# Optimization experiments

Measured on AMD Instinct MI355X. Metric: run time of the kernel, lower is better.

Reference implementation:

```python
import jax, jax.numpy as jnp
import numpy as np

B, C, U, N = 8, 64, 3, 512


def setup_inputs() -> dict:
    key = jax.random.key(0)
    k1, k2, k3, k4 = jax.random.split(key, 4)
    x = jax.random.normal(k1, (B, C, U, N), dtype=jnp.float32)
    # nn.Linear weights [out, in], applied as x @ W.T over channel dim
    s = 1.0 / np.sqrt(C)
    Wq = jax.random.uniform(k2, (C, C), dtype=jnp.float32, minval=-s, maxval=s)
    Wk = jax.random.uniform(k3, (C, C), dtype=jnp.float32, minval=-s, maxval=s)
    Wv = jax.random.uniform(k4, (C, C), dtype=jnp.float32, minval=-s, maxval=s)
    return {"x": x, "Wq": Wq, "Wk": Wk, "Wv": Wv}


def reference(x, Wq, Wk, Wv):
    # VNLinear: Linear over channel dim (dim 1), no bias: out[b,d,u,n] = sum_c x[b,c,u,n] W[d,c]
    def vn_linear(t, W):
        return jnp.einsum('bcun,dc->bdun', t, W)

    q = vn_linear(x, Wq)
    k = vn_linear(x, Wk)
    v = vn_linear(x, Wv)
    scale = x.shape[1] ** (-0.5)  # in_channels^-0.5
    # contraction over tiny vector-neuron dim u=3
    attn_logits = jnp.einsum('bcui,bcuj->bcij', q, k) * scale  # [B,C,N,N]
    attn_weights = jax.nn.softmax(attn_logits, axis=-1)
    out = jnp.einsum('bcij,bcuj->bcui', attn_weights, v)  # [B,C,U,N]
    return x + out
```

## Files before the change

kernel.cpp:

```cpp
#include <hip/hip_runtime.h>

#define BB 8
#define CC 64
#define UU 3
#define NN 512
#define POS (UU * NN)
#define QKV_ELEMS (BB * CC * POS)
#define SCALE2 0.1803368801111793f

__global__ __launch_bounds__(256) void proj_kernel(
    const float* __restrict__ x,
    const float* __restrict__ Wq,
    const float* __restrict__ Wk,
    const float* __restrict__ Wv,
    float* __restrict__ ws)
{
    const int blk   = blockIdx.x;
    const int bd2   = blk / 6;
    const int chunk = blk % 6;
    const int b     = bd2 >> 5;
    const int d0    = (bd2 & 31) * 2;
    const int tid   = threadIdx.x;
    const int p     = chunk * 256 + tid;

    __shared__ float w[6][CC];
    if (tid < 128) {
        int r = tid >> 6, c = tid & 63;
        w[r][c]     = Wq[(d0 + r) * CC + c];
        w[2 + r][c] = Wk[(d0 + r) * CC + c];
        w[4 + r][c] = Wv[(d0 + r) * CC + c];
    }
    __syncthreads();

    const float* xb = x + (size_t)b * CC * POS + p;
    float q0 = 0.f, q1 = 0.f, k0 = 0.f, k1 = 0.f, v0 = 0.f, v1 = 0.f;
    #pragma unroll 8
    for (int c = 0; c < CC; ++c) {
        float xv = xb[c * POS];
        q0 = fmaf(xv, w[0][c], q0);
        q1 = fmaf(xv, w[1][c], q1);
        k0 = fmaf(xv, w[2][c], k0);
        k1 = fmaf(xv, w[3][c], k1);
        v0 = fmaf(xv, w[4][c], v0);
        v1 = fmaf(xv, w[5][c], v1);
    }

    float* qs = ws;
    float* ks = ws + QKV_ELEMS;
    float* vs = ws + 2 * QKV_ELEMS;
    size_t base = (size_t)(b * CC + d0) * POS + p;
    qs[base] = q0 * SCALE2;  qs[base + POS] = q1 * SCALE2;
    ks[base] = k0;           ks[base + POS] = k1;
    vs[base] = v0;           vs[base + POS] = v1;
}

__global__ __launch_bounds__(256) void attn_kernel(
    const float* __restrict__ x,
    const float* __restrict__ ws,
    float* __restrict__ out)
{
    const int blk  = blockIdx.x;
    const int bd   = blk >> 1;
    const int half = blk & 1;
    const int tid  = threadIdx.x;

    __shared__ float ks[UU][NN];
    __shared__ float vs[UU][NN];

    const float* qsg = ws + (size_t)bd * POS;
    const float* ksg = ws + QKV_ELEMS + (size_t)bd * POS;
    const float* vsg = ws + 2 * QKV_ELEMS + (size_t)bd * POS;

    float* ksf = &ks[0][0];
    float* vsf = &vs[0][0];
    for (int t = tid; t < POS; t += 256) {
        ksf[t] = ksg[t];
        vsf[t] = vsg[t];
    }
    __syncthreads();

    const int i  = half * 256 + tid;
    const float q0 = qsg[i];
    const float q1 = qsg[NN + i];
    const float q2 = qsg[2 * NN + i];

    float l = 0.f, a0 = 0.f, a1 = 0.f, a2 = 0.f;
    #pragma unroll 4
    for (int j = 0; j < NN; j += 4) {
        float4 k0 = *(const float4*)&ks[0][j];
        float4 k1 = *(const float4*)&ks[1][j];
        float4 k2 = *(const float4*)&ks[2][j];
        float4 v0 = *(const float4*)&vs[0][j];
        float4 v1 = *(const float4*)&vs[1][j];
        float4 v2 = *(const float4*)&vs[2][j];

        float s0 = fmaf(q0, k0.x, fmaf(q1, k1.x, q2 * k2.x));
        float s1 = fmaf(q0, k0.y, fmaf(q1, k1.y, q2 * k2.y));
        float s2 = fmaf(q0, k0.z, fmaf(q1, k1.z, q2 * k2.z));
        float s3 = fmaf(q0, k0.w, fmaf(q1, k1.w, q2 * k2.w));

        float p0 = __builtin_amdgcn_exp2f(s0);
        float p1 = __builtin_amdgcn_exp2f(s1);
        float p2 = __builtin_amdgcn_exp2f(s2);
        float p3 = __builtin_amdgcn_exp2f(s3);

        l += p0 + p1 + p2 + p3;
        a0 = fmaf(p0, v0.x, fmaf(p1, v0.y, fmaf(p2, v0.z, fmaf(p3, v0.w, a0))));
        a1 = fmaf(p0, v1.x, fmaf(p1, v1.y, fmaf(p2, v1.z, fmaf(p3, v1.w, a1))));
        a2 = fmaf(p0, v2.x, fmaf(p1, v2.y, fmaf(p2, v2.z, fmaf(p3, v2.w, a2))));
    }

    float inv = 1.0f / l;
    const float* xd = x + (size_t)bd * POS;
    float*       od = out + (size_t)bd * POS;
    od[i]           = xd[i]           + a0 * inv;
    od[NN + i]      = xd[NN + i]      + a1 * inv;
    od[2 * NN + i]  = xd[2 * NN + i]  + a2 * inv;
}

__global__ __launch_bounds__(256) void vn_attn_fused(
    const float* __restrict__ x,
    const float* __restrict__ Wq,
    const float* __restrict__ Wk,
    const float* __restrict__ Wv,
    float* __restrict__ out)
{
    const int bd  = blockIdx.x;
    const int b   = bd / CC;
    const int d   = bd % CC;
    const int tid = threadIdx.x;

    __shared__ float wq[CC], wk[CC], wv[CC];
    __shared__ float qs[UU][NN];
    __shared__ float ks[UU][NN];
    __shared__ float vs[UU][NN];

    if (tid < CC) {
        wq[tid] = Wq[d * CC + tid];
        wk[tid] = Wk[d * CC + tid];
        wv[tid] = Wv[d * CC + tid];
    }
    __syncthreads();

    const float* xb = x + (size_t)b * CC * POS;
    for (int p = tid; p < POS; p += 256) {
        float qa = 0.f, ka = 0.f, va = 0.f;
        #pragma unroll 8
        for (int c = 0; c < CC; ++c) {
            float xv = xb[c * POS + p];
            qa = fmaf(xv, wq[c], qa);
            ka = fmaf(xv, wk[c], ka);
            va = fmaf(xv, wv[c], va);
        }
        int u = p >> 9, n = p & (NN - 1);
        qs[u][n] = qa * SCALE2;
        ks[u][n] = ka;
        vs[u][n] = va;
    }
    __syncthreads();

    for (int i = tid; i < NN; i += 256) {
        float q0 = qs[0][i], q1 = qs[1][i], q2 = qs[2][i];
        float l = 0.f, a0 = 0.f, a1 = 0.f, a2 = 0.f;
        for (int j = 0; j < NN; j += 4) {
            float4 k0 = *(const float4*)&ks[0][j];
            float4 k1 = *(const float4*)&ks[1][j];
            float4 k2 = *(const float4*)&ks[2][j];
            float4 v0 = *(const float4*)&vs[0][j];
            float4 v1 = *(const float4*)&vs[1][j];
            float4 v2 = *(const float4*)&vs[2][j];
            float s0 = fmaf(q0, k0.x, fmaf(q1, k1.x, q2 * k2.x));
            float s1 = fmaf(q0, k0.y, fmaf(q1, k1.y, q2 * k2.y));
            float s2 = fmaf(q0, k0.z, fmaf(q1, k1.z, q2 * k2.z));
            float s3 = fmaf(q0, k0.w, fmaf(q1, k1.w, q2 * k2.w));
            float p0 = __builtin_amdgcn_exp2f(s0);
            float p1 = __builtin_amdgcn_exp2f(s1);
            float p2 = __builtin_amdgcn_exp2f(s2);
            float p3 = __builtin_amdgcn_exp2f(s3);
            l += p0 + p1 + p2 + p3;
            a0 = fmaf(p0, v0.x, fmaf(p1, v0.y, fmaf(p2, v0.z, fmaf(p3, v0.w, a0))));
            a1 = fmaf(p0, v1.x, fmaf(p1, v1.y, fmaf(p2, v1.z, fmaf(p3, v1.w, a1))));
            a2 = fmaf(p0, v2.x, fmaf(p1, v2.y, fmaf(p2, v2.z, fmaf(p3, v2.w, a2))));
        }
        float inv = 1.0f / l;
        size_t obase = ((size_t)(b * CC + d) * UU) * NN + i;
        const float* xd = xb + (size_t)d * POS;
        out[obase]          = xd[i]          + a0 * inv;
        out[obase + NN]     = xd[NN + i]     + a1 * inv;
        out[obase + 2 * NN] = xd[2 * NN + i] + a2 * inv;
    }
}

extern "C" void kernel_launch(void* const* d_in, const int* in_sizes, int n_in,
                              void* d_out, int out_size, void* d_ws, size_t ws_size,
                              hipStream_t stream) {
    const float* x  = (const float*)d_in[0];
    const float* Wq = (const float*)d_in[1];
    const float* Wk = (const float*)d_in[2];
    const float* Wv = (const float*)d_in[3];
    float* out = (float*)d_out;

    if (ws_size >= (size_t)3 * QKV_ELEMS * sizeof(float)) {
        float* ws = (float*)d_ws;
        proj_kernel<<<dim3(BB * 32 * 6), dim3(256), 0, stream>>>(x, Wq, Wk, Wv, ws);
        attn_kernel<<<dim3(BB * CC * 2), dim3(256), 0, stream>>>(x, ws, out);
    } else {
        vn_attn_fused<<<dim3(BB * CC), dim3(256), 0, stream>>>(x, Wq, Wk, Wv, out);
    }
}
```

Before: 110.7 us.

## Compute eight output channels per projection block and read K/V directly from global

```diff
diff --git a/kernel.cpp b/kernel.cpp
--- a/kernel.cpp
+++ b/kernel.cpp
@@ -16,42 +16,46 @@
     float* __restrict__ ws)
 {
     const int blk   = blockIdx.x;
-    const int bd2   = blk / 6;
+    const int bg    = blk / 6;
     const int chunk = blk % 6;
-    const int b     = bd2 >> 5;
-    const int d0    = (bd2 & 31) * 2;
+    const int b     = bg >> 3;
+    const int d0    = (bg & 7) * 8;
     const int tid   = threadIdx.x;
     const int p     = chunk * 256 + tid;
 
-    __shared__ float w[6][CC];
-    if (tid < 128) {
-        int r = tid >> 6, c = tid & 63;
-        w[r][c]     = Wq[(d0 + r) * CC + c];
-        w[2 + r][c] = Wk[(d0 + r) * CC + c];
-        w[4 + r][c] = Wv[(d0 + r) * CC + c];
+    __shared__ float w[24][CC];
+    for (int t = tid; t < 24 * CC; t += 256) {
+        int r = t >> 6, c = t & 63;
+        const float* W = (r < 8) ? Wq : (r < 16) ? Wk : Wv;
+        w[r][c] = W[(d0 + (r & 7)) * CC + c];
     }
     __syncthreads();
 
     const float* xb = x + (size_t)b * CC * POS + p;
-    float q0 = 0.f, q1 = 0.f, k0 = 0.f, k1 = 0.f, v0 = 0.f, v1 = 0.f;
-    #pragma unroll 8
+    float qa[8], ka[8], va[8];
+    #pragma unroll
+    for (int r = 0; r < 8; ++r) { qa[r] = 0.f; ka[r] = 0.f; va[r] = 0.f; }
+
     for (int c = 0; c < CC; ++c) {
         float xv = xb[c * POS];
-        q0 = fmaf(xv, w[0][c], q0);
-        q1 = fmaf(xv, w[1][c], q1);
-        k0 = fmaf(xv, w[2][c], k0);
-        k1 = fmaf(xv, w[3][c], k1);
-        v0 = fmaf(xv, w[4][c], v0);
-        v1 = fmaf(xv, w[5][c], v1);
+        #pragma unroll
+        for (int r = 0; r < 8; ++r) {
+            qa[r] = fmaf(xv, w[r][c],      qa[r]);
+            ka[r] = fmaf(xv, w[8 + r][c],  ka[r]);
+            va[r] = fmaf(xv, w[16 + r][c], va[r]);
+        }
     }
 
     float* qs = ws;
     float* ks = ws + QKV_ELEMS;
     float* vs = ws + 2 * QKV_ELEMS;
-    size_t base = (size_t)(b * CC + d0) * POS + p;
-    qs[base] = q0 * SCALE2;  qs[base + POS] = q1 * SCALE2;
-    ks[base] = k0;           ks[base + POS] = k1;
-    vs[base] = v0;           vs[base + POS] = v1;
+    #pragma unroll
+    for (int r = 0; r < 8; ++r) {
+        size_t base = (size_t)(b * CC + d0 + r) * POS + p;
+        qs[base] = qa[r] * SCALE2;
+        ks[base] = ka[r];
+        vs[base] = va[r];
+    }
 }
 
 __global__ __launch_bounds__(256) void attn_kernel(
@@ -63,36 +67,29 @@
     const int bd   = blk >> 1;
     const int half = blk & 1;
     const int tid  = threadIdx.x;
-
-    __shared__ float ks[UU][NN];
-    __shared__ float vs[UU][NN];
-
-    const float* qsg = ws + (size_t)bd * POS;
-    const float* ksg = ws + QKV_ELEMS + (size_t)bd * POS;
-    const float* vsg = ws + 2 * QKV_ELEMS + (size_t)bd * POS;
-
-    float* ksf = &ks[0][0];
-    float* vsf = &vs[0][0];
-    for (int t = tid; t < POS; t += 256) {
-        ksf[t] = ksg[t];
-        vsf[t] = vsg[t];
-    }
-    __syncthreads();
-
-    const int i  = half * 256 + tid;
+    const int i    = half * 256 + tid;
+
+    const float*  qsg = ws + (size_t)bd * POS;
+    const float4* k0p = (const float4*)(ws + QKV_ELEMS     + (size_t)bd * POS);
+    const float4* k1p = k0p + (NN / 4);
+    const float4* k2p = k0p + 2 * (NN / 4);
+    const float4* v0p = (const float4*)(ws + 2 * QKV_ELEMS + (size_t)bd * POS);
+    const float4* v1p = v0p + (NN / 4);
+    const float4* v2p = v0p + 2 * (NN / 4);
+
     const float q0 = qsg[i];
     const float q1 = qsg[NN + i];
     const float q2 = qsg[2 * NN + i];
 
     float l = 0.f, a0 = 0.f, a1 = 0.f, a2 = 0.f;
-    #pragma unroll 4
-    for (int j = 0; j < NN; j += 4) {
-        float4 k0 = *(const float4*)&ks[0][j];
-        float4 k1 = *(const float4*)&ks[1][j];
-        float4 k2 = *(const float4*)&ks[2][j];
-        float4 v0 = *(const float4*)&vs[0][j];
-        float4 v1 = *(const float4*)&vs[1][j];
-        float4 v2 = *(const float4*)&vs[2][j];
+    #pragma unroll 2
+    for (int j4 = 0; j4 < NN / 4; ++j4) {
+        float4 k0 = k0p[j4];
+        float4 k1 = k1p[j4];
+        float4 k2 = k2p[j4];
+        float4 v0 = v0p[j4];
+        float4 v1 = v1p[j4];
+        float4 v2 = v2p[j4];
 
         float s0 = fmaf(q0, k0.x, fmaf(q1, k1.x, q2 * k2.x));
         float s1 = fmaf(q0, k0.y, fmaf(q1, k1.y, q2 * k2.y));
@@ -104,18 +101,18 @@
         float p2 = __builtin_amdgcn_exp2f(s2);
         float p3 = __builtin_amdgcn_exp2f(s3);
 
-        l += p0 + p1 + p2 + p3;
+        l += (p0 + p1) + (p2 + p3);
         a0 = fmaf(p0, v0.x, fmaf(p1, v0.y, fmaf(p2, v0.z, fmaf(p3, v0.w, a0))));
         a1 = fmaf(p0, v1.x, fmaf(p1, v1.y, fmaf(p2, v1.z, fmaf(p3, v1.w, a1))));
         a2 = fmaf(p0, v2.x, fmaf(p1, v2.y, fmaf(p2, v2.z, fmaf(p3, v2.w, a2))));
     }
 
     float inv = 1.0f / l;
-    const float* xd = x + (size_t)bd * POS;
+    const float* xd = x   + (size_t)bd * POS;
     float*       od = out + (size_t)bd * POS;
-    od[i]           = xd[i]           + a0 * inv;
-    od[NN + i]      = xd[NN + i]      + a1 * inv;
-    od[2 * NN + i]  = xd[2 * NN + i]  + a2 * inv;
+    od[i]          = xd[i]          + a0 * inv;
+    od[NN + i]     = xd[NN + i]     + a1 * inv;
+    od[2 * NN + i] = xd[2 * NN + i] + a2 * inv;
 }
 
 __global__ __launch_bounds__(256) void vn_attn_fused(
@@ -202,7 +199,7 @@
 
     if (ws_size >= (size_t)3 * QKV_ELEMS * sizeof(float)) {
         float* ws = (float*)d_ws;
-        proj_kernel<<<dim3(BB * 32 * 6), dim3(256), 0, stream>>>(x, Wq, Wk, Wv, ws);
+        proj_kernel<<<dim3(8 * 8 * 6), dim3(256), 0, stream>>>(x, Wq, Wk, Wv, ws);
         attn_kernel<<<dim3(BB * CC * 2), dim3(256), 0, stream>>>(x, ws, out);
     } else {
         vn_attn_fused<<<dim3(BB * CC), dim3(256), 0, stream>>>(x, Wq, Wk, Wv, out);
```

Result: slower. 124.8 us (+12.7%).

## Split attention key range across thread pairs and read K/V directly from global

Applied to the files above, without the earlier changes.

```diff
diff --git a/kernel.cpp b/kernel.cpp
--- a/kernel.cpp
+++ b/kernel.cpp
@@ -59,40 +59,37 @@
     const float* __restrict__ ws,
     float* __restrict__ out)
 {
-    const int blk  = blockIdx.x;
-    const int bd   = blk >> 1;
-    const int half = blk & 1;
-    const int tid  = threadIdx.x;
-
-    __shared__ float ks[UU][NN];
-    __shared__ float vs[UU][NN];
+    const int blk = blockIdx.x;
+    const int bd  = blk >> 2;
+    const int qb  = blk & 3;
+    const int tid = threadIdx.x;
+    const int i   = qb * 128 + (tid >> 1);
+    const int h   = tid & 1;
 
     const float* qsg = ws + (size_t)bd * POS;
-    const float* ksg = ws + QKV_ELEMS + (size_t)bd * POS;
+    const float* ksg = ws + QKV_ELEMS     + (size_t)bd * POS;
     const float* vsg = ws + 2 * QKV_ELEMS + (size_t)bd * POS;
 
-    float* ksf = &ks[0][0];
-    float* vsf = &vs[0][0];
-    for (int t = tid; t < POS; t += 256) {
-        ksf[t] = ksg[t];
-        vsf[t] = vsg[t];
-    }
-    __syncthreads();
-
-    const int i  = half * 256 + tid;
     const float q0 = qsg[i];
     const float q1 = qsg[NN + i];
     const float q2 = qsg[2 * NN + i];
 
+    const float4* k0p = (const float4*)ksg            + h * 64;
+    const float4* k1p = (const float4*)(ksg + NN)     + h * 64;
+    const float4* k2p = (const float4*)(ksg + 2 * NN) + h * 64;
+    const float4* v0p = (const float4*)vsg            + h * 64;
+    const float4* v1p = (const float4*)(vsg + NN)     + h * 64;
+    const float4* v2p = (const float4*)(vsg + 2 * NN) + h * 64;
+
     float l = 0.f, a0 = 0.f, a1 = 0.f, a2 = 0.f;
-    #pragma unroll 4
-    for (int j = 0; j < NN; j += 4) {
-        float4 k0 = *(const float4*)&ks[0][j];
-        float4 k1 = *(const float4*)&ks[1][j];
-        float4 k2 = *(const float4*)&ks[2][j];
-        float4 v0 = *(const float4*)&vs[0][j];
-        float4 v1 = *(const float4*)&vs[1][j];
-        float4 v2 = *(const float4*)&vs[2][j];
+    #pragma unroll 2
+    for (int t = 0; t < 64; ++t) {
+        float4 k0 = k0p[t];
+        float4 k1 = k1p[t];
+        float4 k2 = k2p[t];
+        float4 v0 = v0p[t];
+        float4 v1 = v1p[t];
+        float4 v2 = v2p[t];
 
         float s0 = fmaf(q0, k0.x, fmaf(q1, k1.x, q2 * k2.x));
         float s1 = fmaf(q0, k0.y, fmaf(q1, k1.y, q2 * k2.y));
@@ -104,18 +101,25 @@
         float p2 = __builtin_amdgcn_exp2f(s2);
         float p3 = __builtin_amdgcn_exp2f(s3);
 
-        l += p0 + p1 + p2 + p3;
+        l += (p0 + p1) + (p2 + p3);
         a0 = fmaf(p0, v0.x, fmaf(p1, v0.y, fmaf(p2, v0.z, fmaf(p3, v0.w, a0))));
         a1 = fmaf(p0, v1.x, fmaf(p1, v1.y, fmaf(p2, v1.z, fmaf(p3, v1.w, a1))));
         a2 = fmaf(p0, v2.x, fmaf(p1, v2.y, fmaf(p2, v2.z, fmaf(p3, v2.w, a2))));
     }
 
-    float inv = 1.0f / l;
-    const float* xd = x + (size_t)bd * POS;
-    float*       od = out + (size_t)bd * POS;
-    od[i]           = xd[i]           + a0 * inv;
-    od[NN + i]      = xd[NN + i]      + a1 * inv;
-    od[2 * NN + i]  = xd[2 * NN + i]  + a2 * inv;
+    l  += __shfl_xor(l,  1);
+    a0 += __shfl_xor(a0, 1);
+    a1 += __shfl_xor(a1, 1);
+    a2 += __shfl_xor(a2, 1);
+
+    if (h == 0) {
+        float inv = 1.0f / l;
+        const float* xd = x   + (size_t)bd * POS;
+        float*       od = out + (size_t)bd * POS;
+        od[i]          = xd[i]          + a0 * inv;
+        od[NN + i]     = xd[NN + i]     + a1 * inv;
+        od[2 * NN + i] = xd[2 * NN + i] + a2 * inv;
+    }
 }
 
 __global__ __launch_bounds__(256) void vn_attn_fused(
@@ -203,7 +207,7 @@
     if (ws_size >= (size_t)3 * QKV_ELEMS * sizeof(float)) {
         float* ws = (float*)d_ws;
         proj_kernel<<<dim3(BB * 32 * 6), dim3(256), 0, stream>>>(x, Wq, Wk, Wv, ws);
-        attn_kernel<<<dim3(BB * CC * 2), dim3(256), 0, stream>>>(x, ws, out);
+        attn_kernel<<<dim3(BB * CC * 4), dim3(256), 0, stream>>>(x, ws, out);
     } else {
         vn_attn_fused<<<dim3(BB * CC), dim3(256), 0, stream>>>(x, Wq, Wk, Wv, out);
     }
```

Result: slower. 239.6 us (+116.5%).
